# Kernel optimization log

Measured on AMD Instinct MI355X. Metric: run time of the kernel, lower is better.

## Reference

```python
import jax, jax.numpy as jnp
import numpy as np
from jax import lax

B, T, HID, NH = 4, 2048, 1024, 16
D = HID // NH
LN_EPS = 1e-5
NORM_EPS = 1e-6


def setup_inputs() -> dict:
    key = jax.random.key(0)
    ks = jax.random.split(key, 3)
    s = 0.02
    return {
        "x": jax.random.normal(ks[0], (B, T, HID), jnp.float32),
        "ln_g": jnp.ones((HID,), jnp.float32),
        "ln_b": jnp.zeros((HID,), jnp.float32),
        "w_qkvb": jax.random.normal(ks[1], (HID, 4 * HID), jnp.float32) * s,
        "b_qkvb": jnp.zeros((4 * HID,), jnp.float32),
        "w_out": jax.random.normal(ks[2], (HID, HID), jnp.float32) * s,
        "b_out": jnp.zeros((HID,), jnp.float32),
    }


def reference(x, ln_g, ln_b, w_qkvb, b_qkvb, w_out, b_out):
    b, t = x.shape[:2]
    # LayerNorm (biased variance, eps=1e-5, matching nn.LayerNorm)
    mu = jnp.mean(x, axis=-1, keepdims=True)
    var = jnp.mean((x - mu) ** 2, axis=-1, keepdims=True)
    normed = (x - mu) * lax.rsqrt(var + LN_EPS) * ln_g + ln_b

    proj = normed @ w_qkvb + b_qkvb  # [B,T,4H]
    q, k, v, beta_pre = jnp.split(proj, 4, axis=-1)
    beta = jax.nn.sigmoid(beta_pre)

    def heads(a):  # [B,T,H] -> [T,B,NH,D] (time-major for scan)
        return a.reshape(b, t, NH, D).transpose(1, 0, 2, 3)

    q, k, v, beta = heads(q), heads(k), heads(v), heads(beta)
    # F.normalize(k, dim=-1, eps=1e-6)
    k = k / jnp.maximum(jnp.linalg.norm(k, axis=-1, keepdims=True), NORM_EPS)

    S0 = jnp.zeros((b, NH, D, D), x.dtype)

    def step(S, inp):
        q_t, k_t, v_t, beta_t = inp  # each [B,NH,D]
        retrieval = jnp.einsum('bhij,bhj->bhi', S, k_t)
        S = S + jnp.einsum('bhi,bhj->bhij', beta_t * (v_t - retrieval), k_t)
        o_t = jnp.einsum('bhij,bhj->bhi', S, q_t)
        return S, o_t

    _, out_t = lax.scan(step, S0, (q, k, v, beta))  # out_t: [T,B,NH,D]
    scan_out = out_t.transpose(1, 0, 2, 3).reshape(b, t, NH * D)
    return x + scan_out @ w_out + b_out
```

## Files before the change

### kernel.cpp

```cpp
#include <hip/hip_runtime.h>
#include <hip/hip_bf16.h>

typedef __attribute__((ext_vector_type(8))) short short8;
typedef __attribute__((ext_vector_type(4))) float f32x4;

#define P72 72

__device__ __forceinline__ unsigned short f2bf(float f) {
    union { float f; unsigned int u; } v; v.f = f;
    unsigned int r = (v.u + 0x7FFFu + ((v.u >> 16) & 1u)) >> 16;
    return (unsigned short)r;
}
__device__ __forceinline__ float bf2f(unsigned short b) {
    union { unsigned int u; float f; } v; v.u = ((unsigned int)b) << 16; return v.f;
}

#define WAVE_SYNC() do { __asm__ volatile("s_waitcnt lgkmcnt(0)" ::: "memory"); \
                         __builtin_amdgcn_sched_barrier(0); } while (0)

#define LGKM_BARRIER() do { __asm__ volatile("s_waitcnt lgkmcnt(0)" ::: "memory"); \
                            __builtin_amdgcn_s_barrier(); \
                            __builtin_amdgcn_sched_barrier(0); } while (0)

#define ASYNC16(G, L) __builtin_amdgcn_global_load_lds( \
    (const __attribute__((address_space(1))) void*)(G), \
    (__attribute__((address_space(3))) void*)(L), 16, 0, 0)

__global__ __launch_bounds__(256) void ln_wqt_kernel(
    const float* __restrict__ x, const float* __restrict__ g,
    const float* __restrict__ bv_, unsigned short* __restrict__ out,
    const float* __restrict__ w_qkvb, unsigned short* __restrict__ WQT)
{
    __shared__ float pool[32 * 33];
    const int tid = threadIdx.x;
    if (blockIdx.x < 8192) {
        const int row = blockIdx.x;
        const float4 v = ((const float4*)(x + (size_t)row * 1024))[tid];
        float s  = v.x + v.y + v.z + v.w;
        float s2 = v.x * v.x + v.y * v.y + v.z * v.z + v.w * v.w;
#pragma unroll
        for (int off = 1; off < 64; off <<= 1) {
            s  += __shfl_xor(s, off);
            s2 += __shfl_xor(s2, off);
        }
        const int wv = tid >> 6;
        if ((tid & 63) == 0) { pool[wv] = s; pool[4 + wv] = s2; }
        __syncthreads();
        s  = pool[0] + pool[1] + pool[2] + pool[3];
        s2 = pool[4] + pool[5] + pool[6] + pool[7];
        const float mu  = s * (1.0f / 1024.0f);
        const float var = s2 * (1.0f / 1024.0f) - mu * mu;
        const float inv = rsqrtf(var + 1e-5f);
        const float4 gv = ((const float4*)g)[tid];
        const float4 bb = ((const float4*)bv_)[tid];
        ushort4 o;
        o.x = f2bf((v.x - mu) * inv * gv.x + bb.x);
        o.y = f2bf((v.y - mu) * inv * gv.y + bb.y);
        o.z = f2bf((v.z - mu) * inv * gv.z + bb.z);
        o.w = f2bf((v.w - mu) * inv * gv.w + bb.w);
        *(ushort4*)(out + (size_t)row * 1024 + tid * 4) = o;
    } else {
        const int blk = blockIdx.x - 8192;
        const int c0 = (blk & 127) * 32, r0 = (blk >> 7) * 32;
        const int tx = tid & 31, ty = tid >> 5;
#pragma unroll
        for (int yy = 0; yy < 32; yy += 8)
            pool[(ty + yy) * 33 + tx] = w_qkvb[(size_t)(r0 + ty + yy) * 4096 + c0 + tx];
        __syncthreads();
#pragma unroll
        for (int yy = 0; yy < 32; yy += 8)
            WQT[(size_t)(c0 + ty + yy) * 1024 + r0 + tx] = f2bf(pool[tx * 33 + ty + yy]);
    }
}

__global__ __launch_bounds__(256) void gemm128(
    const unsigned short* __restrict__ A, const unsigned short* __restrict__ Bt,
    const float* __restrict__ bias, int K, int N, int mode, int n0_off,
    const float* __restrict__ resid, float* __restrict__ outf,
    unsigned short* __restrict__ qo, unsigned short* __restrict__ ko,
    unsigned short* __restrict__ vo, unsigned short* __restrict__ bo)
{
    __shared__ __align__(16) unsigned short SMEM[24576];
    const int tid = threadIdx.x;
    const int nwg = (int)(gridDim.x * gridDim.y);
    const int flat = (int)(blockIdx.y * gridDim.x + blockIdx.x);
    const int id2 = (flat & 7) * (nwg >> 3) + (flat >> 3);
    const int M0 = (id2 / (int)gridDim.x) * 128;
    const int N0 = (id2 % (int)gridDim.x) * 128 + n0_off;
    const int lane = tid & 63;
    const int w = tid >> 6, wr = w >> 1, wc = w & 1;
    const int r15 = lane & 15, kg = lane >> 4;
    const int lr = lane >> 2, lc = (lane & 3) * 8;

    const unsigned short* Arow0 = A  + (size_t)(M0 + w * 16 + lr) * K + lc;
    const unsigned short* Arow1 = A  + (size_t)(M0 + 64 + w * 16 + lr) * K + lc;
    const unsigned short* Brow0 = Bt + (size_t)(N0 + w * 16 + lr) * K + lc;
    const unsigned short* Brow1 = Bt + (size_t)(N0 + 64 + w * 16 + lr) * K + lc;

    f32x4 acc[4][4] = {};

    ASYNC16(Arow0, &SMEM[(w * 16) * 32]);
    ASYNC16(Arow1, &SMEM[(64 + w * 16) * 32]);
    ASYNC16(Brow0, &SMEM[12288 + (w * 16) * 32]);
    ASYNC16(Brow1, &SMEM[12288 + (64 + w * 16) * 32]);
    if (32 < K) {
        ASYNC16(Arow0 + 32, &SMEM[4096 + (w * 16) * 32]);
        ASYNC16(Arow1 + 32, &SMEM[4096 + (64 + w * 16) * 32]);
        ASYNC16(Brow0 + 32, &SMEM[12288 + 4096 + (w * 16) * 32]);
        ASYNC16(Brow1 + 32, &SMEM[12288 + 4096 + (64 + w * 16) * 32]);
    }

    int cur = 0;
    for (int k0 = 0; k0 < K; k0 += 32) {
        if (k0 + 64 < K) {
            int n2 = cur + 2; if (n2 >= 3) n2 -= 3;
            const int nb = n2 * 4096;
            ASYNC16(Arow0 + k0 + 64, &SMEM[nb + (w * 16) * 32]);
            ASYNC16(Arow1 + k0 + 64, &SMEM[nb + (64 + w * 16) * 32]);
            ASYNC16(Brow0 + k0 + 64, &SMEM[12288 + nb + (w * 16) * 32]);
            ASYNC16(Brow1 + k0 + 64, &SMEM[12288 + nb + (64 + w * 16) * 32]);
            __asm__ volatile("s_waitcnt vmcnt(8)" ::: "memory");
        } else if (k0 + 32 < K) {
            __asm__ volatile("s_waitcnt vmcnt(4)" ::: "memory");
        } else {
            __asm__ volatile("s_waitcnt vmcnt(0)" ::: "memory");
        }
        __builtin_amdgcn_s_barrier();
        __builtin_amdgcn_sched_barrier(0);
        const int cb = cur * 4096;
        short8 af[4], bf[4];
#pragma unroll
        for (int m = 0; m < 4; m++)
            af[m] = *(const short8*)&SMEM[cb + (wr * 64 + m * 16 + r15) * 32 + kg * 8];
#pragma unroll
        for (int n = 0; n < 4; n++)
            bf[n] = *(const short8*)&SMEM[12288 + cb + (wc * 64 + n * 16 + r15) * 32 + kg * 8];
#pragma unroll
        for (int m = 0; m < 4; m++)
#pragma unroll
            for (int n = 0; n < 4; n++)
                acc[m][n] = __builtin_amdgcn_mfma_f32_16x16x32_bf16(af[m], bf[n], acc[m][n], 0, 0, 0);
        __builtin_amdgcn_sched_barrier(0);
        __builtin_amdgcn_s_barrier();
        cur += 1; if (cur >= 3) cur = 0;
    }

    float bias_r[4];
#pragma unroll
    for (int n = 0; n < 4; n++) bias_r[n] = bias[N0 + wc * 64 + n * 16 + r15];

    if (mode == 0) {
        const int sec = N0 >> 10;
        const int hA = (N0 & 1023) >> 6;
        unsigned short* arr = (sec == 0) ? qo : (sec == 1) ? ko : (sec == 2) ? vo : bo;
#pragma unroll
        for (int p = 0; p < 2; ++p) {
            __syncthreads();
            if (wr == p) {
#pragma unroll
                for (int m = 0; m < 4; m++)
#pragma unroll
                    for (int n = 0; n < 4; n++)
#pragma unroll
                        for (int j = 0; j < 4; j++) {
                            float val = acc[m][n][j] + bias_r[n];
                            if (sec == 3) val = 1.0f / (1.0f + expf(-val));
                            SMEM[(m * 16 + kg * 4 + j) * 136 + wc * 64 + n * 16 + r15] = f2bf(val);
                        }
            }
            __syncthreads();
            const int tl = tid >> 2, sg = tid & 3;
            const int gm = M0 + p * 64 + tl;
            const int b = gm >> 11, t = gm & 2047;
            const int h = hA + (sg >> 1), d0 = (sg & 1) * 32;
            const int colbase = sg * 32;
            const size_t dst = ((size_t)(b * 16 + h) * 2048 + t) * 64 + d0;
#pragma unroll
            for (int i = 0; i < 4; i++) {
                uint4 v = *(const uint4*)&SMEM[tl * 136 + colbase + i * 8];
                *(uint4*)(arr + dst + i * 8) = v;
            }
        }
    } else {
        float* stf = (float*)SMEM;
#pragma unroll
        for (int p = 0; p < 4; ++p) {
            __syncthreads();
            if (wr == (p >> 1)) {
#pragma unroll
                for (int mm = 0; mm < 2; mm++)
#pragma unroll
                    for (int n = 0; n < 4; n++)
#pragma unroll
                        for (int j = 0; j < 4; j++)
                            stf[(mm * 16 + kg * 4 + j) * 132 + wc * 64 + n * 16 + r15] =
                                acc[(p & 1) * 2 + mm][n][j] + bias_r[n];
            }
            __syncthreads();
            const int rl = tid >> 3, sg = (tid & 7) * 16;
            const size_t rowo = (size_t)(M0 + p * 32 + rl) * N + N0 + sg;
#pragma unroll
            for (int i = 0; i < 4; i++) {
                float4 v = *(const float4*)&stf[rl * 132 + sg + i * 4];
                float4 r = *(const float4*)(resid + rowo + i * 4);
                v.x += r.x; v.y += r.y; v.z += r.z; v.w += r.w;
                *(float4*)(outf + rowo + i * 4) = v;
            }
        }
    }
}

__global__ __launch_bounds__(256) void prep_kernel(
    const unsigned short* __restrict__ Kpre, const unsigned short* __restrict__ Vin,
    const unsigned short* __restrict__ Bin,
    unsigned short* __restrict__ Kb, unsigned short* __restrict__ A0g,
    float* __restrict__ A0Dg, unsigned short* __restrict__ KTg,
    unsigned short* __restrict__ VTg, unsigned short* __restrict__ BTg)
{
    __shared__ __align__(16) unsigned short Ks[64 * P72];
    __shared__ __align__(16) unsigned short Vs[64 * P72];
    __shared__ __align__(16) unsigned short Bs[64 * P72];
    __shared__ __align__(16) unsigned short Os[64 * P72];
    const int cid = blockIdx.x, tid = threadIdx.x;
    const size_t gbase = (size_t)cid * 4096;
    const int r0 = tid >> 2, c0 = (tid & 3) * 16;
    {
        uint4 k0 = *(const uint4*)(Kpre + gbase + r0 * 64 + c0), k1 = *(const uint4*)(Kpre + gbase + r0 * 64 + c0 + 8);
        uint4 v0 = *(const uint4*)(Vin + gbase + r0 * 64 + c0),  v1 = *(const uint4*)(Vin + gbase + r0 * 64 + c0 + 8);
        uint4 b0 = *(const uint4*)(Bin + gbase + r0 * 64 + c0),  b1 = *(const uint4*)(Bin + gbase + r0 * 64 + c0 + 8);
        *(uint4*)&Ks[r0 * P72 + c0] = k0; *(uint4*)&Ks[r0 * P72 + c0 + 8] = k1;
        *(uint4*)&Vs[r0 * P72 + c0] = v0; *(uint4*)&Vs[r0 * P72 + c0 + 8] = v1;
        *(uint4*)&Bs[r0 * P72 + c0] = b0; *(uint4*)&Bs[r0 * P72 + c0 + 8] = b1;
    }
    __syncthreads();
    {
        const int row = tid >> 2, seg = tid & 3;
        float v[16]; float ss = 0.f;
#pragma unroll
        for (int q = 0; q < 16; q++) { v[q] = bf2f(Ks[row * P72 + seg * 16 + q]); ss = fmaf(v[q], v[q], ss); }
        ss += __shfl_xor(ss, 1); ss += __shfl_xor(ss, 2);
        const float inv = 1.0f / fmaxf(sqrtf(ss), 1e-6f);
        unsigned short t16[16];
#pragma unroll
        for (int q = 0; q < 16; q++) t16[q] = f2bf(v[q] * inv);
        *(uint4*)&Ks[row * P72 + seg * 16]     = *(uint4*)&t16[0];
        *(uint4*)&Ks[row * P72 + seg * 16 + 8] = *(uint4*)&t16[8];
        *(uint4*)(Kb + gbase + row * 64 + seg * 16)     = *(uint4*)&t16[0];
        *(uint4*)(Kb + gbase + row * 64 + seg * 16 + 8) = *(uint4*)&t16[8];
    }
    __syncthreads();
    const int lane = tid & 63, w = tid >> 6;
    const int r15 = lane & 15, kg = lane >> 4;
    f32x4 acc[4] = {{0,0,0,0},{0,0,0,0},{0,0,0,0},{0,0,0,0}};
#pragma unroll
    for (int ks = 0; ks < 2; ks++) {
        short8 afr = *(const short8*)&Ks[(w * 16 + r15) * P72 + ks * 32 + kg * 8];
#pragma unroll
        for (int n = 0; n < 4; n++) {
            short8 bfr = *(const short8*)&Ks[(n * 16 + r15) * P72 + ks * 32 + kg * 8];
            acc[n] = __builtin_amdgcn_mfma_f32_16x16x32_bf16(afr, bfr, acc[n], 0, 0, 0);
        }
    }
#pragma unroll
    for (int n = 0; n < 4; n++) {
#pragma unroll
        for (int j = 0; j < 4; j++) {
            const int s = w * 16 + kg * 4 + j, r = n * 16 + r15;
            Os[s * P72 + r] = (r < s) ? f2bf(acc[n][j]) : (unsigned short)0;
        }
        if (n == w) {
            float4 d;
            d.x = (r15 < kg * 4 + 0) ? acc[n][0] : 0.f;
            d.y = (r15 < kg * 4 + 1) ? acc[n][1] : 0.f;
            d.z = (r15 < kg * 4 + 2) ? acc[n][2] : 0.f;
            d.w = (r15 < kg * 4 + 3) ? acc[n][3] : 0.f;
            *(float4*)(A0Dg + (size_t)cid * 1024 + w * 256 + r15 * 16 + kg * 4) = d;
        }
    }
    __syncthreads();
    {
        uint4 x0 = *(const uint4*)&Os[r0 * P72 + c0];
        uint4 x1 = *(const uint4*)&Os[r0 * P72 + c0 + 8];
        *(uint4*)(A0g + gbase + r0 * 64 + c0) = x0;
        *(uint4*)(A0g + gbase + r0 * 64 + c0 + 8) = x1;
    }
    {
        const int d = tid >> 2, s0 = (tid & 3) * 16;
        unsigned short tk[16], tv[16], tb[16];
#pragma unroll
        for (int k = 0; k < 16; k++) {
            tk[k] = Ks[(s0 + k) * P72 + d];
            tv[k] = Vs[(s0 + k) * P72 + d];
            tb[k] = Bs[(s0 + k) * P72 + d];
        }
        *(uint4*)(KTg + gbase + (size_t)d * 64 + s0)     = *(uint4*)&tk[0];
        *(uint4*)(KTg + gbase + (size_t)d * 64 + s0 + 8) = *(uint4*)&tk[8];
        *(uint4*)(VTg + gbase + (size_t)d * 64 + s0)     = *(uint4*)&tv[0];
        *(uint4*)(VTg + gbase + (size_t)d * 64 + s0 + 8) = *(uint4*)&tv[8];
        *(uint4*)(BTg + gbase + (size_t)d * 64 + s0)     = *(uint4*)&tb[0];
        *(uint4*)(BTg + gbase + (size_t)d * 64 + s0 + 8) = *(uint4*)&tb[8];
    }
}

__global__ __launch_bounds__(256, 1) void fused_scan_kernel(
    const unsigned short* __restrict__ A0g, const unsigned short* __restrict__ Kb,
    const unsigned short* __restrict__ KTg, const float* __restrict__ A0Dg,
    const unsigned short* __restrict__ VTg, const unsigned short* __restrict__ BTg,
    unsigned short* __restrict__ Scg, unsigned short* __restrict__ UTg,
    const unsigned short* __restrict__ NORM, const unsigned short* __restrict__ WQT,
    const float* __restrict__ bias, unsigned short* __restrict__ qo,
    const float* __restrict__ w_out, unsigned short* __restrict__ WOT)
{
    __shared__ __align__(16) unsigned char POOL[120832];
    unsigned short* us = (unsigned short*)POOL;
    const int tid = threadIdx.x;

    if (blockIdx.x < 64) {
        unsigned short* sK  = us;
        unsigned short* sKT = us + 9216;
        unsigned short* sA0 = us + 18432;
        unsigned short* sVT = us + 27648;
        unsigned short* sBT = us + 36864;
        float* sA0D = (float*)(POOL + 92160);
        unsigned short* Sbf = us + 51200;
        unsigned short* UTs = us + 55808;

        const int bh = blockIdx.x;
        const int lane = tid & 63, w = tid >> 6;
        const int r15 = lane & 15, kg = lane >> 4;
        const int sr = tid >> 2, sc = (tid & 3) * 16;
        const int qr = 16 * w + (lane >> 2), qc = (lane & 3) * 16;
        const size_t base0 = (size_t)bh * 32 * 4096;
        const size_t baseD = (size_t)bh * 32 * 1024;
        const int dOff = (w * 16 + (sr & 15)) * 20 + (tid & 3) * 4;

        f32x4 Sreg[4] = {};
        uint4 g[10]; float4 gD;

        const uint4 z4 = {0u, 0u, 0u, 0u};
        *(uint4*)&Sbf[sr * P72 + sc] = z4;
        *(uint4*)&Sbf[sr * P72 + sc + 8] = z4;
        {
            const size_t gb = base0 + sr * 64 + sc;
            g[0] = *(const uint4*)(Kb  + gb); g[1] = *(const uint4*)(Kb  + gb + 8);
            g[2] = *(const uint4*)(KTg + gb); g[3] = *(const uint4*)(KTg + gb + 8);
            g[4] = *(const uint4*)(A0g + gb); g[5] = *(const uint4*)(A0g + gb + 8);
            g[6] = *(const uint4*)(VTg + gb); g[7] = *(const uint4*)(VTg + gb + 8);
            g[8] = *(const uint4*)(BTg + gb); g[9] = *(const uint4*)(BTg + gb + 8);
            gD   = *(const float4*)(A0Dg + baseD + tid * 4);
            *(uint4*)&sK [sr * P72 + sc] = g[0]; *(uint4*)&sK [sr * P72 + sc + 8] = g[1];
            *(uint4*)&sKT[sr * P72 + sc] = g[2]; *(uint4*)&sKT[sr * P72 + sc + 8] = g[3];
            *(uint4*)&sA0[sr * P72 + sc] = g[4]; *(uint4*)&sA0[sr * P72 + sc + 8] = g[5];
            *(uint4*)&sVT[sr * P72 + sc] = g[6]; *(uint4*)&sVT[sr * P72 + sc + 8] = g[7];
            *(uint4*)&sBT[sr * P72 + sc] = g[8]; *(uint4*)&sBT[sr * P72 + sc + 8] = g[9];
            *(float4*)&sA0D[dOff] = gD;
        }

#pragma unroll 1
        for (int c = 0; c < 32; ++c) {
            const int cur = c & 1, nxt = cur ^ 1;
            LGKM_BARRIER();
            if (c < 31) {
                const size_t gb = base0 + (size_t)(c + 1) * 4096 + sr * 64 + sc;
                g[0] = *(const uint4*)(Kb  + gb); g[1] = *(const uint4*)(Kb  + gb + 8);
                g[2] = *(const uint4*)(KTg + gb); g[3] = *(const uint4*)(KTg + gb + 8);
                g[4] = *(const uint4*)(A0g + gb); g[5] = *(const uint4*)(A0g + gb + 8);
                g[6] = *(const uint4*)(VTg + gb); g[7] = *(const uint4*)(VTg + gb + 8);
                g[8] = *(const uint4*)(BTg + gb); g[9] = *(const uint4*)(BTg + gb + 8);
                gD   = *(const float4*)(A0Dg + baseD + (size_t)(c + 1) * 1024 + tid * 4);
            }
            const unsigned short* KsC  = &sK [cur * 4608];
            const unsigned short* KTsC = &sKT[cur * 4608];
            const unsigned short* A0C  = &sA0[cur * 4608];
            const unsigned short* VTC  = &sVT[cur * 4608];
            const unsigned short* BTC  = &sBT[cur * 4608];
            const float*          A0DC = &sA0D[cur * 1280];

            *(uint4*)&UTs[(16 * w + r15) * P72 + kg * 16] = z4;
            *(uint4*)&UTs[(16 * w + r15) * P72 + kg * 16 + 8] = z4;

            {
                uint4 a = *(const uint4*)&Sbf[qr * P72 + qc];
                uint4 b2 = *(const uint4*)&Sbf[qr * P72 + qc + 8];
                const unsigned FL = 0x80008000u;
                a.x ^= FL; a.y ^= FL; a.z ^= FL; a.w ^= FL;
                b2.x ^= FL; b2.y ^= FL; b2.z ^= FL; b2.w ^= FL;
                const size_t so = base0 + (size_t)c * 4096 + qr * 64 + qc;
                *(uint4*)(Scg + so) = a;
                *(uint4*)(Scg + so + 8) = b2;
            }

            f32x4 y[4];
#pragma unroll
            for (int st = 0; st < 4; st++) {
                ushort4 vv = *(const ushort4*)&VTC[(16 * w + r15) * P72 + st * 16 + kg * 4];
                y[st][0] = bf2f(vv.x); y[st][1] = bf2f(vv.y);
                y[st][2] = bf2f(vv.z); y[st][3] = bf2f(vv.w);
            }
#pragma unroll
            for (int ks = 0; ks < 2; ks++) {
                short8 bfr = *(const short8*)&Sbf[(16 * w + r15) * P72 + ks * 32 + kg * 8];
#pragma unroll
                for (int st = 0; st < 4; st++) {
                    short8 afr = *(const short8*)&KsC[(st * 16 + r15) * P72 + ks * 32 + kg * 8];
                    y[st] = __builtin_amdgcn_mfma_f32_16x16x32_bf16(afr, bfr, y[st], 0, 0, 0);
                }
            }

#pragma unroll
            for (int b = 0; b < 4; b++) {
                if (b > 0) {
                    WAVE_SYNC();
                    f32x4 corr = {};
                    {
                        short8 afr = *(const short8*)&A0C[(b * 16 + r15) * P72 + kg * 8];
                        short8 bfr = *(const short8*)&UTs[(16 * w + r15) * P72 + kg * 8];
                        corr = __builtin_amdgcn_mfma_f32_16x16x32_bf16(afr, bfr, corr, 0, 0, 0);
                    }
                    if (b == 3) {
                        short8 afr = *(const short8*)&A0C[(b * 16 + r15) * P72 + 32 + kg * 8];
                        short8 bfr = *(const short8*)&UTs[(16 * w + r15) * P72 + 32 + kg * 8];
                        corr = __builtin_amdgcn_mfma_f32_16x16x32_bf16(afr, bfr, corr, 0, 0, 0);
                    }
                    y[b] = y[b] - corr;
                }
                ushort4 bt4 = *(const ushort4*)&BTC[(16 * w + r15) * P72 + b * 16 + kg * 4];
                const float bta0 = bf2f(bt4.x), bta1 = bf2f(bt4.y);
                const float bta2 = bf2f(bt4.z), bta3 = bf2f(bt4.w);
                float us0 = 0.f, us1 = 0.f, us2 = 0.f, us3 = 0.f;
#pragma unroll
                for (int own = 0; own < 4; own++) {
                    const f32x4 c40 = *(const f32x4*)&A0DC[(b * 16 + own * 4 + 0) * 20 + kg * 4];
                    const f32x4 c41 = *(const f32x4*)&A0DC[(b * 16 + own * 4 + 1) * 20 + kg * 4];
                    const f32x4 c42 = *(const f32x4*)&A0DC[(b * 16 + own * 4 + 2) * 20 + kg * 4];
                    const f32x4 c43 = *(const f32x4*)&A0DC[(b * 16 + own * 4 + 3) * 20 + kg * 4];
                    if (kg == own) {
                        us0 = bta0 * y[b][0];
                        us1 = bta1 * (y[b][1] - c40[1] * us0);
                        us2 = bta2 * (y[b][2] - c40[2] * us0 - c41[2] * us1);
                        us3 = bta3 * (y[b][3] - c40[3] * us0 - c41[3] * us1 - c42[3] * us2);
                    }
                    const int src = own * 16 + r15;
                    const float u0 = __shfl(us0, src), u1 = __shfl(us1, src);
                    const float u2 = __shfl(us2, src), u3 = __shfl(us3, src);
                    if (kg > own)
                        y[b] = y[b] - (c40 * u0 + c41 * u1 + c42 * u2 + c43 * u3);
                }
                ushort4 up;
                up.x = f2bf(us0); up.y = f2bf(us1); up.z = f2bf(us2); up.w = f2bf(us3);
                *(ushort4*)&UTs[(16 * w + r15) * P72 + b * 16 + kg * 4] = up;
            }
            WAVE_SYNC();

            {
                uint4 a = *(const uint4*)&UTs[qr * P72 + qc];
                uint4 b2 = *(const uint4*)&UTs[qr * P72 + qc + 8];
                const size_t so = base0 + (size_t)c * 4096 + qr * 64 + qc;
                *(uint4*)(UTg + so) = a;
                *(uint4*)(UTg + so + 8) = b2;
            }

#pragma unroll
            for (int ks = 0; ks < 2; ks++) {
                short8 afr = *(const short8*)&UTs[(16 * w + r15) * P72 + ks * 32 + kg * 8];
#pragma unroll
                for (int n = 0; n < 4; n++) {
                    short8 bfr = *(const short8*)&KTsC[(n * 16 + r15) * P72 + ks * 32 + kg * 8];
                    Sreg[n] = __builtin_amdgcn_mfma_f32_16x16x32_bf16(afr, bfr, Sreg[n], 0, 0, 0);
                }
            }
#pragma unroll
            for (int n = 0; n < 4; n++)
#pragma unroll
                for (int jj = 0; jj < 4; jj++)
                    Sbf[(16 * w + kg * 4 + jj) * P72 + n * 16 + r15] = f2bf(-Sreg[n][jj]);

            if (c < 31) {
                *(uint4*)&sK [nxt * 4608 + sr * P72 + sc] = g[0]; *(uint4*)&sK [nxt * 4608 + sr * P72 + sc + 8] = g[1];
                *(uint4*)&sKT[nxt * 4608 + sr * P72 + sc] = g[2]; *(uint4*)&sKT[nxt * 4608 + sr * P72 + sc + 8] = g[3];
                *(uint4*)&sA0[nxt * 4608 + sr * P72 + sc] = g[4]; *(uint4*)&sA0[nxt * 4608 + sr * P72 + sc + 8] = g[5];
                *(uint4*)&sVT[nxt * 4608 + sr * P72 + sc] = g[6]; *(uint4*)&sVT[nxt * 4608 + sr * P72 + sc + 8] = g[7];
                *(uint4*)&sBT[nxt * 4608 + sr * P72 + sc] = g[8]; *(uint4*)&sBT[nxt * 4608 + sr * P72 + sc + 8] = g[9];
                *(float4*)&sA0D[nxt * 1280 + dOff] = gD;
            }
        }
    } else if (blockIdx.x < 64 + 512) {
        unsigned short* SMEM = us;
        const int blk = blockIdx.x - 64;
        const int M0 = (blk >> 3) * 128, N0 = (blk & 7) * 128;
        const int K = 1024;
        const int lane = tid & 63;
        const int w = tid >> 6, wr = w >> 1, wc = w & 1;
        const int r15 = lane & 15, kg = lane >> 4;
        const int lr = lane >> 2, lc = (lane & 3) * 8;

        const unsigned short* Arow0 = NORM + (size_t)(M0 + w * 16 + lr) * K + lc;
        const unsigned short* Arow1 = NORM + (size_t)(M0 + 64 + w * 16 + lr) * K + lc;
        const unsigned short* Brow0 = WQT + (size_t)(N0 + w * 16 + lr) * K + lc;
        const unsigned short* Brow1 = WQT + (size_t)(N0 + 64 + w * 16 + lr) * K + lc;

        f32x4 acc[4][4] = {};

        ASYNC16(Arow0, &SMEM[(w * 16) * 32]);
        ASYNC16(Arow1, &SMEM[(64 + w * 16) * 32]);
        ASYNC16(Brow0, &SMEM[8192 + (w * 16) * 32]);
        ASYNC16(Brow1, &SMEM[8192 + (64 + w * 16) * 32]);

        int cur = 0;
        for (int k0 = 0; k0 < K; k0 += 32) {
            if (k0 + 32 < K) {
                const int nb = (cur ^ 1) * 4096;
                ASYNC16(Arow0 + k0 + 32, &SMEM[nb + (w * 16) * 32]);
                ASYNC16(Arow1 + k0 + 32, &SMEM[nb + (64 + w * 16) * 32]);
                ASYNC16(Brow0 + k0 + 32, &SMEM[8192 + nb + (w * 16) * 32]);
                ASYNC16(Brow1 + k0 + 32, &SMEM[8192 + nb + (64 + w * 16) * 32]);
                __asm__ volatile("s_waitcnt vmcnt(4)" ::: "memory");
            } else {
                __asm__ volatile("s_waitcnt vmcnt(0)" ::: "memory");
            }
            __builtin_amdgcn_s_barrier();
            __builtin_amdgcn_sched_barrier(0);
            const int cb = cur * 4096;
            short8 af[4], bf[4];
#pragma unroll
            for (int m = 0; m < 4; m++)
                af[m] = *(const short8*)&SMEM[cb + (wr * 64 + m * 16 + r15) * 32 + kg * 8];
#pragma unroll
            for (int n = 0; n < 4; n++)
                bf[n] = *(const short8*)&SMEM[8192 + cb + (wc * 64 + n * 16 + r15) * 32 + kg * 8];
#pragma unroll
            for (int m = 0; m < 4; m++)
#pragma unroll
                for (int n = 0; n < 4; n++)
                    acc[m][n] = __builtin_amdgcn_mfma_f32_16x16x32_bf16(af[m], bf[n], acc[m][n], 0, 0, 0);
            __builtin_amdgcn_sched_barrier(0);
            __builtin_amdgcn_s_barrier();
            cur ^= 1;
        }

        float bias_r[4];
#pragma unroll
        for (int n = 0; n < 4; n++) bias_r[n] = bias[N0 + wc * 64 + n * 16 + r15];
        const int hA = N0 >> 6;
#pragma unroll
        for (int p = 0; p < 2; ++p) {
            __syncthreads();
            if (wr == p) {
#pragma unroll
                for (int m = 0; m < 4; m++)
#pragma unroll
                    for (int n = 0; n < 4; n++)
#pragma unroll
                        for (int j = 0; j < 4; j++)
                            SMEM[(m * 16 + kg * 4 + j) * 136 + wc * 64 + n * 16 + r15] =
                                f2bf(acc[m][n][j] + bias_r[n]);
            }
            __syncthreads();
            const int tl = tid >> 2, sg = tid & 3;
            const int gm = M0 + p * 64 + tl;
            const int b = gm >> 11, t = gm & 2047;
            const int h = hA + (sg >> 1), d0 = (sg & 1) * 32;
            const int colbase = sg * 32;
            const size_t dst = ((size_t)(b * 16 + h) * 2048 + t) * 64 + d0;
#pragma unroll
            for (int i = 0; i < 4; i++) {
                uint4 v = *(const uint4*)&SMEM[tl * 136 + colbase + i * 8];
                *(uint4*)(qo + dst + i * 8) = v;
            }
        }
    } else {
        float* tile = (float*)POOL;
        const int blk = blockIdx.x - 64 - 512;
        const int c0 = (blk & 31) * 32, r0 = (blk >> 5) * 32;
        const int tx = tid & 31, ty = tid >> 5;
#pragma unroll
        for (int yy = 0; yy < 32; yy += 8)
            tile[(ty + yy) * 33 + tx] = w_out[(size_t)(r0 + ty + yy) * 1024 + c0 + tx];
        __syncthreads();
#pragma unroll
        for (int yy = 0; yy < 32; yy += 8)
            WOT[(size_t)(c0 + ty + yy) * 1024 + r0 + tx] = f2bf(tile[tx * 33 + ty + yy]);
    }
}

__global__ __launch_bounds__(256) void out_kernel(
    const unsigned short* __restrict__ Qb, const unsigned short* __restrict__ Kb,
    const unsigned short* __restrict__ Scg, const unsigned short* __restrict__ UTg,
    unsigned short* __restrict__ attn)
{
    __shared__ __align__(16) unsigned short Qs[64 * P72];
    __shared__ __align__(16) unsigned short Kbs[64 * P72];
    __shared__ __align__(16) unsigned short Scs[64 * P72];
    __shared__ __align__(16) unsigned short UTss[64 * P72];
    __shared__ __align__(16) unsigned short Ms[64 * P72];
    __shared__ __align__(16) unsigned short Osb[64 * P72];
    const int blk = blockIdx.x, tid = threadIdx.x;
    const int bh = blk >> 5, cc = blk & 31;
    const size_t gbase = (size_t)blk * 4096;
    const int lane = tid & 63, w = tid >> 6;
    const int r15 = lane & 15, kg = lane >> 4;
    {
        const int r0 = tid >> 2, c0 = (tid & 3) * 16;
        uint4 q0 = *(const uint4*)(Qb + gbase + r0 * 64 + c0),  q1 = *(const uint4*)(Qb + gbase + r0 * 64 + c0 + 8);
        uint4 k0 = *(const uint4*)(Kb + gbase + r0 * 64 + c0),  k1 = *(const uint4*)(Kb + gbase + r0 * 64 + c0 + 8);
        uint4 s0 = *(const uint4*)(Scg + gbase + r0 * 64 + c0), s1 = *(const uint4*)(Scg + gbase + r0 * 64 + c0 + 8);
        uint4 u0 = *(const uint4*)(UTg + gbase + r0 * 64 + c0), u1 = *(const uint4*)(UTg + gbase + r0 * 64 + c0 + 8);
        *(uint4*)&Qs [r0 * P72 + c0] = q0; *(uint4*)&Qs [r0 * P72 + c0 + 8] = q1;
        *(uint4*)&Kbs[r0 * P72 + c0] = k0; *(uint4*)&Kbs[r0 * P72 + c0 + 8] = k1;
        *(uint4*)&Scs[r0 * P72 + c0] = s0; *(uint4*)&Scs[r0 * P72 + c0 + 8] = s1;
        *(uint4*)&UTss[r0 * P72 + c0] = u0; *(uint4*)&UTss[r0 * P72 + c0 + 8] = u1;
    }
    __syncthreads();
    {
        f32x4 accm[4] = {{0,0,0,0},{0,0,0,0},{0,0,0,0},{0,0,0,0}};
#pragma unroll
        for (int ks = 0; ks < 2; ks++) {
            short8 afr = *(const short8*)&Qs[(w * 16 + r15) * P72 + ks * 32 + kg * 8];
#pragma unroll
            for (int n = 0; n < 4; n++) {
                short8 bfr = *(const short8*)&Kbs[(n * 16 + r15) * P72 + ks * 32 + kg * 8];
                accm[n] = __builtin_amdgcn_mfma_f32_16x16x32_bf16(afr, bfr, accm[n], 0, 0, 0);
            }
        }
#pragma unroll
        for (int n = 0; n < 4; n++)
#pragma unroll
            for (int j = 0; j < 4; j++) {
                const int t = w * 16 + kg * 4 + j, s = n * 16 + r15;
                Ms[t * P72 + s] = (s <= t) ? f2bf(accm[n][j]) : (unsigned short)0;
            }
    }
    __syncthreads();
    {
        f32x4 acc[4] = {{0,0,0,0},{0,0,0,0},{0,0,0,0},{0,0,0,0}};
#pragma unroll
        for (int ks = 0; ks < 2; ks++) {
            short8 afr = *(const short8*)&Qs[(w * 16 + r15) * P72 + ks * 32 + kg * 8];
#pragma unroll
            for (int n = 0; n < 4; n++) {
                short8 bfr = *(const short8*)&Scs[(n * 16 + r15) * P72 + ks * 32 + kg * 8];
                acc[n] = __builtin_amdgcn_mfma_f32_16x16x32_bf16(afr, bfr, acc[n], 0, 0, 0);
            }
        }
#pragma unroll
        for (int ks = 0; ks < 2; ks++) {
            short8 afr = *(const short8*)&Ms[(w * 16 + r15) * P72 + ks * 32 + kg * 8];
#pragma unroll
            for (int n = 0; n < 4; n++) {
                short8 bfr = *(const short8*)&UTss[(n * 16 + r15) * P72 + ks * 32 + kg * 8];
                acc[n] = __builtin_amdgcn_mfma_f32_16x16x32_bf16(afr, bfr, acc[n], 0, 0, 0);
            }
        }
#pragma unroll
        for (int n = 0; n < 4; n++)
#pragma unroll
            for (int j = 0; j < 4; j++) {
                const int t = w * 16 + kg * 4 + j, i = n * 16 + r15;
                Osb[t * P72 + i] = f2bf(acc[n][j]);
            }
    }
    __syncthreads();
    {
        const int b = bh >> 4, h = bh & 15;
        const int t = tid >> 2, i0 = (tid & 3) * 16;
        uint4 o0 = *(const uint4*)&Osb[t * P72 + i0];
        uint4 o1 = *(const uint4*)&Osb[t * P72 + i0 + 8];
        unsigned short* dst = attn + ((size_t)(b * 2048 + cc * 64 + t)) * 1024 + h * 64 + i0;
        *(uint4*)dst = o0;
        *(uint4*)(dst + 8) = o1;
    }
}

extern "C" void kernel_launch(void* const* d_in, const int* in_sizes, int n_in,
                              void* d_out, int out_size, void* d_ws, size_t ws_size,
                              hipStream_t stream)
{
    const float* x      = (const float*)d_in[0];
    const float* ln_g   = (const float*)d_in[1];
    const float* ln_b   = (const float*)d_in[2];
    const float* w_qkvb = (const float*)d_in[3];
    const float* b_qkvb = (const float*)d_in[4];
    const float* w_out  = (const float*)d_in[5];
    const float* b_out  = (const float*)d_in[6];
    float* out = (float*)d_out;

    char* ws = (char*)d_ws;
    size_t off = 0;
    auto alloc = [&](size_t bytes) -> char* {
        char* p = ws + off;
        off = (off + bytes + 255) & ~(size_t)255;
        return p;
    };
    const size_t TOK = 64ull * 2048 * 64;
    unsigned short* WQT  = (unsigned short*)alloc(4096ull * 1024 * 2);
    unsigned short* WOT  = (unsigned short*)alloc(1024ull * 1024 * 2);
    unsigned short* NORM = (unsigned short*)alloc(TOK * 2 * 2);
    unsigned short* Qb   = (unsigned short*)alloc(TOK * 2);
    unsigned short* Kpre = (unsigned short*)alloc(TOK * 2);
    unsigned short* Kb   = (unsigned short*)alloc(TOK * 2);
    unsigned short* KTb  = (unsigned short*)alloc(TOK * 2);
    unsigned short* Vb   = (unsigned short*)alloc(TOK * 2);
    unsigned short* Bb   = (unsigned short*)alloc(TOK * 2);
    unsigned short* A0   = (unsigned short*)alloc(TOK * 2);
    unsigned short* Sc   = (unsigned short*)alloc(TOK * 2);
    unsigned short* UT   = (unsigned short*)alloc(TOK * 2);
    float*          A0D  = (float*)alloc(2048ull * 1024 * 4);
    unsigned short* ATTN = NORM;
    unsigned short* VTb  = Vb;
    unsigned short* BTb  = Bb;

    hipLaunchKernelGGL(ln_wqt_kernel, dim3(8192 + 4096), dim3(256), 0, stream,
                       x, ln_g, ln_b, NORM, w_qkvb, WQT);
    hipLaunchKernelGGL(gemm128, dim3(24, 64), dim3(256), 0, stream,
                       NORM, WQT, b_qkvb, 1024, 4096, 0, 1024,
                       (const float*)nullptr, (float*)nullptr, Qb, Kpre, Vb, Bb);
    hipLaunchKernelGGL(prep_kernel, dim3(2048), dim3(256), 0, stream,
                       Kpre, Vb, Bb, Kb, A0, A0D, KTb, VTb, BTb);
    hipLaunchKernelGGL(fused_scan_kernel, dim3(64 + 512 + 1024), dim3(256), 0, stream,
                       A0, Kb, KTb, A0D, VTb, BTb, Sc, UT,
                       NORM, WQT, b_qkvb, Qb, w_out, WOT);
    hipLaunchKernelGGL(out_kernel, dim3(2048), dim3(256), 0, stream, Qb, Kb, Sc, UT, ATTN);
    hipLaunchKernelGGL(gemm128, dim3(8, 64), dim3(256), 0, stream,
                       ATTN, WOT, b_out, 1024, 1024, 1, 0,
                       x, out, (unsigned short*)nullptr, (unsigned short*)nullptr,
                       (unsigned short*)nullptr, (unsigned short*)nullptr);
}
```

Before: 322.0 us.

## Replace QKVB projection GEMM with 256x128-tile, 512-thread triple-buffered kernel

Adds a new gemm256 kernel that computes 256x128 output tiles with 8 waves and a three-stage LDS ring of async global-to-LDS loads. Each K-step is split into four MFMA phases, with prefetch loads interleaved between them and s_setprio raising wave priority during the MFMA phases. The goal is more operand reuse per LDS load and better overlap of memory traffic with matrix math in the projection GEMM. The epilogue still applies the sigmoid for the beta section and writes head-major bf16. In exchange it uses a large LDS footprint (about 144KB) and fewer, larger workgroups, which may cut occupancy and leave the grid less balanced.

```diff
diff --git a/kernel.cpp b/kernel.cpp
--- a/kernel.cpp
+++ b/kernel.cpp
@@ -206,6 +206,164 @@
                 v.x += r.x; v.y += r.y; v.z += r.z; v.w += r.w;
                 *(float4*)(outf + rowo + i * 4) = v;
             }
+        }
+    }
+}
+
+__global__ __launch_bounds__(512, 2) void gemm256(
+    const unsigned short* __restrict__ A, const unsigned short* __restrict__ Bt,
+    const float* __restrict__ bias, int K, int n0_off,
+    unsigned short* __restrict__ qo, unsigned short* __restrict__ ko,
+    unsigned short* __restrict__ vo, unsigned short* __restrict__ bo)
+{
+    __shared__ __align__(16) unsigned short SMEM[73728];
+    const int tid = threadIdx.x;
+    const int nwg = (int)(gridDim.x * gridDim.y);
+    const int flat = (int)(blockIdx.y * gridDim.x + blockIdx.x);
+    const int id2 = (flat & 7) * (nwg >> 3) + (flat >> 3);
+    const int M0 = (id2 / (int)gridDim.x) * 256;
+    const int N0 = (id2 % (int)gridDim.x) * 128 + n0_off;
+
+    const int lane = tid & 63, wv = tid >> 6;
+    const int wr = wv >> 2, wc = wv & 3;
+    const int r15 = lane & 15, kg = lane >> 4;
+    const int swz = r15 & 7;
+
+    const int srow = lane >> 3;
+    const int schk = (lane & 7) ^ srow;
+    const unsigned short* Asrc = A  + (size_t)(M0 + wv * 8 + srow) * K + schk * 8;
+    const unsigned short* Bsrc = Bt + (size_t)(N0 + wv * 8 + srow) * K + schk * 8;
+
+    float bias_r[2];
+    bias_r[0] = bias[N0 + wc * 32 + r15];
+    bias_r[1] = bias[N0 + wc * 32 + 16 + r15];
+    __builtin_amdgcn_sched_barrier(0);
+
+    auto stageA = [&](int b_, int ko_, int i_) {
+        ASYNC16(Asrc + (size_t)i_ * 64 * K + ko_,
+                &SMEM[b_ * 24576 + (i_ * 64 + wv * 8) * 64]);
+    };
+    auto stageB = [&](int b_, int ko_, int i_) {
+        ASYNC16(Bsrc + (size_t)i_ * 64 * K + ko_,
+                &SMEM[b_ * 24576 + 16384 + (i_ * 64 + wv * 8) * 64]);
+    };
+
+#pragma unroll
+    for (int i = 0; i < 4; i++) stageA(0, 0, i);
+    stageB(0, 0, 0); stageB(0, 0, 1);
+#pragma unroll
+    for (int i = 0; i < 4; i++) stageA(1, 64, i);
+    stageB(1, 64, 0); stageB(1, 64, 1);
+
+    f32x4 acc[8][2] = {};
+
+#define PH_PRE() do { __builtin_amdgcn_s_barrier(); \
+                      __asm__ volatile("s_waitcnt lgkmcnt(0)" ::: "memory"); \
+                      __builtin_amdgcn_sched_barrier(0); \
+                      __builtin_amdgcn_s_setprio(1); } while (0)
+#define PH_POST() do { __builtin_amdgcn_s_setprio(0); \
+                       __builtin_amdgcn_sched_barrier(0); \
+                       __builtin_amdgcn_s_barrier(); } while (0)
+
+    const int NT = K >> 6;
+    int cur = 0;
+    for (int t = 0; t < NT; ++t) {
+        if (t + 1 < NT) { __asm__ volatile("s_waitcnt vmcnt(6)" ::: "memory"); }
+        else            { __asm__ volatile("s_waitcnt vmcnt(0)" ::: "memory"); }
+        __builtin_amdgcn_s_barrier();
+        __builtin_amdgcn_sched_barrier(0);
+
+        const unsigned short* Ab = &SMEM[cur * 24576];
+        const unsigned short* Bb = &SMEM[cur * 24576 + 16384];
+        int nb = cur + 2; if (nb >= 3) nb -= 3;
+        const int nko = (t + 2) * 64;
+        const bool pf = (t + 2 < NT);
+
+        short8 af[4], bf[2];
+#pragma unroll
+        for (int m = 0; m < 4; m++)
+            af[m] = *(const short8*)&Ab[(wr * 128 + m * 16 + r15) * 64 + (kg ^ swz) * 8];
+#pragma unroll
+        for (int n = 0; n < 2; n++)
+            bf[n] = *(const short8*)&Bb[(wc * 32 + n * 16 + r15) * 64 + (kg ^ swz) * 8];
+        if (pf) { stageA(nb, nko, 0); stageA(nb, nko, 1); }
+        PH_PRE();
+#pragma unroll
+        for (int m = 0; m < 4; m++)
+#pragma unroll
+            for (int n = 0; n < 2; n++)
+                acc[m][n] = __builtin_amdgcn_mfma_f32_16x16x32_bf16(af[m], bf[n], acc[m][n], 0, 0, 0);
+        PH_POST();
+#pragma unroll
+        for (int m = 0; m < 4; m++)
+            af[m] = *(const short8*)&Ab[(wr * 128 + (m + 4) * 16 + r15) * 64 + (kg ^ swz) * 8];
+        if (pf) { stageA(nb, nko, 2); stageA(nb, nko, 3); }
+        PH_PRE();
+#pragma unroll
+        for (int m = 0; m < 4; m++)
+#pragma unroll
+            for (int n = 0; n < 2; n++)
+                acc[m + 4][n] = __builtin_amdgcn_mfma_f32_16x16x32_bf16(af[m], bf[n], acc[m + 4][n], 0, 0, 0);
+        PH_POST();
+#pragma unroll
+        for (int m = 0; m < 4; m++)
+            af[m] = *(const short8*)&Ab[(wr * 128 + m * 16 + r15) * 64 + ((4 + kg) ^ swz) * 8];
+#pragma unroll
+        for (int n = 0; n < 2; n++)
+            bf[n] = *(const short8*)&Bb[(wc * 32 + n * 16 + r15) * 64 + ((4 + kg) ^ swz) * 8];
+        if (pf) { stageB(nb, nko, 0); stageB(nb, nko, 1); }
+        PH_PRE();
+#pragma unroll
+        for (int m = 0; m < 4; m++)
+#pragma unroll
+            for (int n = 0; n < 2; n++)
+                acc[m][n] = __builtin_amdgcn_mfma_f32_16x16x32_bf16(af[m], bf[n], acc[m][n], 0, 0, 0);
+        PH_POST();
+#pragma unroll
+        for (int m = 0; m < 4; m++)
+            af[m] = *(const short8*)&Ab[(wr * 128 + (m + 4) * 16 + r15) * 64 + ((4 + kg) ^ swz) * 8];
+        PH_PRE();
+#pragma unroll
+        for (int m = 0; m < 4; m++)
+#pragma unroll
+            for (int n = 0; n < 2; n++)
+                acc[m + 4][n] = __builtin_amdgcn_mfma_f32_16x16x32_bf16(af[m], bf[n], acc[m + 4][n], 0, 0, 0);
+        __builtin_amdgcn_s_setprio(0);
+        __builtin_amdgcn_sched_barrier(0);
+
+        cur += 1; if (cur >= 3) cur = 0;
+    }
+#undef PH_PRE
+#undef PH_POST
+
+    const int sec = N0 >> 10;
+    const int hA = (N0 & 1023) >> 6;
+    unsigned short* arr = (sec == 0) ? qo : (sec == 1) ? ko : (sec == 2) ? vo : bo;
+#pragma unroll
+    for (int p = 0; p < 2; ++p) {
+        __syncthreads();
+        if (wr == p) {
+#pragma unroll
+            for (int m = 0; m < 8; m++)
+#pragma unroll
+                for (int n = 0; n < 2; n++)
+#pragma unroll
+                    for (int j = 0; j < 4; j++) {
+                        float val = acc[m][n][j] + bias_r[n];
+                        if (sec == 3) val = 1.0f / (1.0f + expf(-val));
+                        SMEM[(m * 16 + kg * 4 + j) * 136 + wc * 32 + n * 16 + r15] = f2bf(val);
+                    }
+        }
+        __syncthreads();
+        const int row = tid >> 2, sg = tid & 3;
+        const int gm = M0 + p * 128 + row;
+        const int b = gm >> 11, tt = gm & 2047;
+        const int h = hA + (sg >> 1), d0 = (sg & 1) * 32;
+        const size_t dst = ((size_t)(b * 16 + h) * 2048 + tt) * 64 + d0;
+#pragma unroll
+        for (int i = 0; i < 4; i++) {
+            uint4 v = *(const uint4*)&SMEM[row * 136 + sg * 32 + i * 8];
+            *(uint4*)(arr + dst + i * 8) = v;
         }
     }
 }
@@ -711,9 +869,8 @@
 
     hipLaunchKernelGGL(ln_wqt_kernel, dim3(8192 + 4096), dim3(256), 0, stream,
                        x, ln_g, ln_b, NORM, w_qkvb, WQT);
-    hipLaunchKernelGGL(gemm128, dim3(24, 64), dim3(256), 0, stream,
-                       NORM, WQT, b_qkvb, 1024, 4096, 0, 1024,
-                       (const float*)nullptr, (float*)nullptr, Qb, Kpre, Vb, Bb);
+    hipLaunchKernelGGL(gemm256, dim3(24, 32), dim3(512), 0, stream,
+                       NORM, WQT, b_qkvb, 1024, 1024, Qb, Kpre, Vb, Bb);
     hipLaunchKernelGGL(prep_kernel, dim3(2048), dim3(256), 0, stream,
                        Kpre, Vb, Bb, Kb, A0, A0D, KTb, VTb, BTb);
     hipLaunchKernelGGL(fused_scan_kernel, dim3(64 + 512 + 1024), dim3(256), 0, stream,
```

Measured after the change: 330.3 us. +2.6%, slower.
